# Optimization experiments

Measured on AMD Instinct MI355X. Metric: run time of the kernel, lower is better.

## Reference

```python
import jax, jax.numpy as jnp
import numpy as np

N_NODES = 32768
N_EDGES = 524288
NODE_DIM = 128
HIDDEN = 256
EDGE_DIM = 32


def setup_inputs() -> dict:
    key = jax.random.key(0)
    ks = jax.random.split(key, 12)
    s = 0.05
    return {
        "h": jax.random.normal(ks[0], (N_NODES, NODE_DIM), jnp.float32),
        "x": jax.random.normal(ks[1], (N_NODES, 3), jnp.float32) * 10.0,
        "edge_index": jax.random.randint(ks[2], (2, N_EDGES), 0, N_NODES, dtype=jnp.int32).astype(jnp.int64),
        "edge_dist": jax.random.uniform(ks[3], (N_EDGES,), jnp.float32) * 15.0,
        # edge_mlp: Linear(1, edge_dim) -> SiLU -> Linear(edge_dim, edge_dim)
        "We1": jax.random.normal(ks[4], (1, EDGE_DIM), jnp.float32) * s,
        "be1": jnp.zeros((EDGE_DIM,), jnp.float32),
        "We2": jax.random.normal(ks[5], (EDGE_DIM, EDGE_DIM), jnp.float32) * s,
        "be2": jnp.zeros((EDGE_DIM,), jnp.float32),
        # node_mlp: Linear(2*node+edge, hidden) -> SiLU -> Linear(hidden, node)
        "Wn1": jax.random.normal(ks[6], (2 * NODE_DIM + EDGE_DIM, HIDDEN), jnp.float32) * s,
        "bn1": jnp.zeros((HIDDEN,), jnp.float32),
        "Wn2": jax.random.normal(ks[7], (HIDDEN, NODE_DIM), jnp.float32) * s,
        "bn2": jnp.zeros((NODE_DIM,), jnp.float32),
        # coord_mlp: Linear(2*node+edge, hidden) -> SiLU -> Linear(hidden, 1, bias=False)
        "Wc1": jax.random.normal(ks[8], (2 * NODE_DIM + EDGE_DIM, HIDDEN), jnp.float32) * s,
        "bc1": jnp.zeros((HIDDEN,), jnp.float32),
        "Wc2": jax.random.normal(ks[9], (HIDDEN, 1), jnp.float32) * s,
    }


def reference(h, x, edge_index, edge_dist,
              We1, be1, We2, be2,
              Wn1, bn1, Wn2, bn2,
              Wc1, bc1, Wc2):
    src, dst = edge_index[0], edge_index[1]
    n_nodes = h.shape[0]

    # edge_mlp on scalar distances -> [E, edge_dim]
    edge_attr = jax.nn.silu(edge_dist[:, None] @ We1 + be1) @ We2 + be2

    # per-edge message input: [E, 2*node_dim + edge_dim]
    m_input = jnp.concatenate([h[src], h[dst], edge_attr], axis=-1)

    # node messages and scatter-add onto destination nodes
    m = jax.nn.silu(m_input @ Wn1 + bn1) @ Wn2 + bn2          # [E, node_dim]
    h_agg = jax.ops.segment_sum(m, dst, num_segments=n_nodes)  # [N, node_dim]

    # equivariant coordinate update along normalized edge direction
    coord_weight = jax.nn.silu(m_input @ Wc1 + bc1) @ Wc2      # [E, 1]
    dir_vec = x[src] - x[dst]                                  # [E, 3]
    dir_len = jnp.maximum(jnp.linalg.norm(dir_vec, axis=-1, keepdims=True), 1e-8)
    coord_update = coord_weight * (dir_vec / dir_len)          # [E, 3]
    x_agg = jax.ops.segment_sum(coord_update, dst, num_segments=n_nodes)

    return h + h_agg, x + x_agg
```

## Files before the change

### kernel.cpp

```cpp
#include <hip/hip_runtime.h>
#include <math.h>

#define N_NODES 32768
#define N_EDGES 524288
#define NODE_DIM 128
#define HIDDEN 256
#define EDGE_DIM 32
#define TE 64
#define ASTR 296
#define HSTR 264
#define MSTR 132

typedef __attribute__((ext_vector_type(8))) short bf16x8;
typedef __attribute__((ext_vector_type(16))) float f32x16;

__device__ __forceinline__ float silu_f(float v) {
    float e = __expf(-v);
    return v * __builtin_amdgcn_rcpf(1.0f + e);
}

__device__ __forceinline__ unsigned short f2bf_rne(float f) {
    union { float f; unsigned int u; } v; v.f = f;
    return (unsigned short)((v.u + 0x7fffu + ((v.u >> 16) & 1u)) >> 16);
}
__device__ __forceinline__ unsigned int pk_rne(float a, float b) {
    return (unsigned int)f2bf_rne(a) | ((unsigned int)f2bf_rne(b) << 16);
}
__device__ __forceinline__ unsigned int pkbf(float a, float b) {
    union { float f; unsigned int u; } ua, ub; ua.f = a; ub.f = b;
    return __builtin_amdgcn_perm(ub.u + 0x8000u, ua.u + 0x8000u, 0x07060302u);
}
__device__ __forceinline__ unsigned short f2bf_hu(float f) {
    union { float f; unsigned int u; } v; v.f = f;
    return (unsigned short)((v.u + 0x8000u) >> 16);
}

__device__ __forceinline__ int detect_is64(const void* ei, int t) {
    const unsigned int* ew = (const unsigned int*)ei;
    unsigned int hiw = ew[2 * (t & 63) + 1];
    return (__ballot(hiw != 0u) == 0ULL) ? 1 : 0;
}

#define WS_BIAS_OFF 1024
#define WS_W1S_OFF  69632
#define WS_W2S_OFF  364544
#define WS_CNT_OFF  430080
#define WS_CUR_OFF  561152
#define WS_PERM_OFF 692224
#define WS_PART_OFF 2789376
#define WS_HBF_OFF  2790400
#define WS_HBF_END  (WS_HBF_OFF + N_NODES * NODE_DIM * 2)

#define SEG_CNT  32768
#define SEG_W1S  147456
#define SEG_W2S  32768
#define SEG_BIAS 512
#define SEG_OUT  1073152
#define SEG_HBF  524288
#define PREP_TOT (SEG_CNT + SEG_W1S + SEG_W2S + SEG_BIAS + SEG_OUT + SEG_HBF)

__global__ void prep_all_kernel(const float* __restrict__ h, const float* __restrict__ x,
                                const float* __restrict__ We2, const float* __restrict__ be2,
                                const float* __restrict__ Wn1, const float* __restrict__ bn1,
                                const float* __restrict__ Wn2,
                                const float* __restrict__ Wc1, const float* __restrict__ bc1,
                                float* __restrict__ out, float* __restrict__ biasC,
                                unsigned short* __restrict__ W1s, unsigned short* __restrict__ W2s,
                                int* __restrict__ counts, unsigned short* __restrict__ hbf) {
    int i = blockIdx.x * 256 + threadIdx.x;
    if (i < SEG_CNT) { counts[i] = 0; return; }
    i -= SEG_CNT;
    if (i < SEG_W1S) {
        int jj = i & 7, ln = (i >> 3) & 63, rest = i >> 9;
        int step = rest % 18, tile = rest / 18;
        int n = tile * 32 + (ln & 31);
        int k = step * 16 + ((ln >> 5) * 8) + jj;
        float v;
        if (k < 256) {
            v = (n < 256) ? Wn1[k * 256 + n] : Wc1[k * 256 + (n - 256)];
        } else {
            int j = k - 256;
            float s = 0.0f;
            #pragma unroll 8
            for (int q = 0; q < 32; ++q)
                s += We2[j * 32 + q] * ((n < 256) ? Wn1[(256 + q) * 256 + n]
                                                  : Wc1[(256 + q) * 256 + (n - 256)]);
            v = s;
        }
        W1s[i] = f2bf_rne(v);
        return;
    }
    i -= SEG_W1S;
    if (i < SEG_W2S) {
        int jj = i & 7, ln = (i >> 3) & 63, rest = i >> 9;
        int step = rest & 15, tile = rest >> 4;
        int d = tile * 32 + (ln & 31);
        int k = step * 16 + ((ln >> 5) * 8) + jj;
        W2s[i] = f2bf_rne(Wn2[k * 128 + d]);
        return;
    }
    i -= SEG_W2S;
    if (i < SEG_BIAS) {
        int n = i;
        float s = (n < 256) ? bn1[n] : bc1[n - 256];
        #pragma unroll 8
        for (int q = 0; q < 32; ++q)
            s += be2[q] * ((n < 256) ? Wn1[(256 + q) * 256 + n]
                                     : Wc1[(256 + q) * 256 + (n - 256)]);
        biasC[n] = s;
        return;
    }
    i -= SEG_BIAS;
    if (i < SEG_OUT) {
        const int NH4 = N_NODES * NODE_DIM / 4;
        const float4* h4 = (const float4*)h;
        const float4* x4 = (const float4*)x;
        ((float4*)out)[i] = (i < NH4) ? h4[i] : x4[i - NH4];
        return;
    }
    i -= SEG_OUT;
    if (hbf != nullptr && i < SEG_HBF) {
        const float4* p = (const float4*)&h[i * 8];
        float4 v0 = p[0], v1 = p[1];
        uint4 o = make_uint4(pk_rne(v0.x, v0.y), pk_rne(v0.z, v0.w),
                             pk_rne(v1.x, v1.y), pk_rne(v1.z, v1.w));
        *(uint4*)&hbf[i * 8] = o;
    }
}

__global__ void hist_kernel(const void* __restrict__ ei, int* __restrict__ counts) {
    int is64 = detect_is64(ei, threadIdx.x);
    int e = blockIdx.x * 256 + threadIdx.x;
    int dst = is64 ? (int)((const long long*)ei)[N_EDGES + e]
                   : ((const int*)ei)[N_EDGES + e];
    atomicAdd(&counts[dst], 1);
}

__global__ __launch_bounds__(256)
void scanA_kernel(const int* __restrict__ counts, int* __restrict__ partials) {
    __shared__ int red[256];
    const int t = threadIdx.x;
    const int b = blockIdx.x;
    red[t] = counts[b * 256 + t];
    __syncthreads();
    #pragma unroll
    for (int s = 128; s > 0; s >>= 1) {
        if (t < s) red[t] += red[t + s];
        __syncthreads();
    }
    if (t == 0) partials[b] = red[0];
}

__global__ __launch_bounds__(256)
void scanC_kernel(const int* __restrict__ counts, const int* __restrict__ partials,
                  int* __restrict__ cursor) {
    __shared__ int pb[128];
    __shared__ int loc[256];
    const int t = threadIdx.x;
    const int b = blockIdx.x;
    if (t < 128) pb[t] = partials[t];
    int c = counts[b * 256 + t];
    loc[t] = c;
    __syncthreads();
    if (t == 0) {
        int s = 0;
        for (int j = 0; j < 128; ++j) { int v = pb[j]; pb[j] = s; s += v; }
    }
    #pragma unroll
    for (int d = 1; d < 256; d <<= 1) {
        int v = (t >= d) ? loc[t - d] : 0;
        __syncthreads();
        loc[t] += v;
        __syncthreads();
    }
    cursor[b * 256 + t] = pb[b] + loc[t] - c;
}

__global__ void place_kernel(const void* __restrict__ ei,
                             int* __restrict__ cursor, int* __restrict__ perm) {
    int is64 = detect_is64(ei, threadIdx.x);
    int e = blockIdx.x * 256 + threadIdx.x;
    int dst = is64 ? (int)((const long long*)ei)[N_EDGES + e]
                   : ((const int*)ei)[N_EDGES + e];
    int pos = atomicAdd(&cursor[dst], 1);
    perm[pos] = e;
}

__global__ __launch_bounds__(512, 4)
void egnn_mfma_kernel(const float* __restrict__ h, const float* __restrict__ x,
                      const void* __restrict__ ei, const float* __restrict__ dist,
                      const float* __restrict__ We1, const float* __restrict__ be1,
                      const float* __restrict__ bn2, const float* __restrict__ Wc2,
                      const float* __restrict__ biasC,
                      const unsigned short* __restrict__ W1s,
                      const unsigned short* __restrict__ W2s,
                      const int* __restrict__ perm,
                      const unsigned short* __restrict__ hbf,
                      float* __restrict__ out)
{
    __shared__ unsigned short smA[TE * ASTR];
    __shared__ int sidx[TE], didx[TE], eidx[TE];
    __shared__ float cw_s[TE];
    __shared__ float cxyz[3 * TE];

    unsigned short* smH = smA;
    float* smM = (float*)smA;

    const int t = threadIdx.x;
    const int lane = t & 63;
    const int wv = t >> 6;
    const int lo = lane & 31;
    const int hi = lane >> 5;
    const int ebase = blockIdx.x * TE;
    const int is64 = detect_is64(ei, t);

    if (t < 2 * TE) {
        int e = t & (TE - 1);
        int eid = perm[ebase + e];
        int which = t >> 6;
        long long pos = (long long)which * N_EDGES + eid;
        int idx = is64 ? (int)((const long long*)ei)[pos] : ((const int*)ei)[pos];
        if (which == 0) { sidx[e] = idx; eidx[e] = eid; }
        else didx[e] = idx;
        if (t < TE) cw_s[t] = 0.0f;
    }
    __syncthreads();

    if (hbf != nullptr) {
        #pragma unroll
        for (int it = 0; it < 4; ++it) {
            int id = it * 512 + t;
            int g = id & 15;
            int half = (id >> 4) & 1;
            int e = id >> 5;
            int node = half ? didx[e] : sidx[e];
            uint4 v = *(const uint4*)&hbf[node * NODE_DIM + 8 * g];
            *(uint4*)&smA[e * ASTR + half * NODE_DIM + 8 * g] = v;
        }
    } else {
        #pragma unroll
        for (int it = 0; it < 4; ++it) {
            int id = it * 512 + t;
            int g8 = id & 15;
            int half = (id >> 4) & 1;
            int e = id >> 5;
            int node = half ? didx[e] : sidx[e];
            const float4* p = (const float4*)&h[node * NODE_DIM + 8 * g8];
            float4 v0 = p[0], v1 = p[1];
            unsigned int a0 = pkbf(v0.x, v0.y), a1 = pkbf(v0.z, v0.w);
            unsigned int a2 = pkbf(v1.x, v1.y), a3 = pkbf(v1.z, v1.w);
            *(uint4*)&smA[e * ASTR + half * NODE_DIM + 8 * g8] = make_uint4(a0, a1, a2, a3);
        }
    }
    {
        int e = t >> 3;
        int j4 = (t & 7) * 4;
        float d = dist[eidx[e]];
        float s0 = silu_f(d * We1[j4 + 0] + be1[j4 + 0]);
        float s1 = silu_f(d * We1[j4 + 1] + be1[j4 + 1]);
        float s2 = silu_f(d * We1[j4 + 2] + be1[j4 + 2]);
        float s3 = silu_f(d * We1[j4 + 3] + be1[j4 + 3]);
        *(uint2*)&smA[e * ASTR + 2 * NODE_DIM + j4] = make_uint2(pkbf(s0, s1), pkbf(s2, s3));
    }
    __syncthreads();

    f32x16 a00, a01, a10, a11;
    {
        int nb = wv * 64 + lo;
        float b0 = biasC[nb], b1 = biasC[nb + 32];
        #pragma unroll
        for (int r = 0; r < 16; ++r) { a00[r] = b0; a01[r] = b1; a10[r] = b0; a11[r] = b1; }
    }
    {
        const int aoff0 = lo * ASTR + hi * 8;
        const int aoff1 = (32 + lo) * ASTR + hi * 8;
        const int TS = 18 * 64 * 8;
        const int base = ((wv * 2 * 18) * 64 + lane) * 8;
        bf16x8 b0s[3], b1s[3];
        b0s[0] = *(const bf16x8*)&W1s[base];
        b1s[0] = *(const bf16x8*)&W1s[base + TS];
        b0s[1] = *(const bf16x8*)&W1s[base + 512];
        b1s[1] = *(const bf16x8*)&W1s[base + 512 + TS];
        #pragma unroll
        for (int step = 0; step < 18; ++step) {
            const int cur = step % 3;
            if (step + 2 < 18) {
                const int pf = (step + 2) % 3;
                b0s[pf] = *(const bf16x8*)&W1s[base + (step + 2) * 512];
                b1s[pf] = *(const bf16x8*)&W1s[base + (step + 2) * 512 + TS];
            }
            bf16x8 f0 = *(const bf16x8*)&smA[aoff0 + step * 16];
            bf16x8 f1 = *(const bf16x8*)&smA[aoff1 + step * 16];
            a00 = __builtin_amdgcn_mfma_f32_32x32x16_bf16(f0, b0s[cur], a00, 0, 0, 0);
            a10 = __builtin_amdgcn_mfma_f32_32x32x16_bf16(f1, b0s[cur], a10, 0, 0, 0);
            a01 = __builtin_amdgcn_mfma_f32_32x32x16_bf16(f0, b1s[cur], a01, 0, 0, 0);
            a11 = __builtin_amdgcn_mfma_f32_32x32x16_bf16(f1, b1s[cur], a11, 0, 0, 0);
        }
    }
    __syncthreads();

    const int rowbase = 4 * hi;
    if (wv < 4) {
        int jb = wv * 64 + lo;
        #pragma unroll
        for (int r = 0; r < 16; ++r) {
            int er = (r & 3) + 8 * (r >> 2) + rowbase;
            unsigned short* row0 = &smH[er * HSTR + jb];
            unsigned short* row1 = &smH[(er + 32) * HSTR + jb];
            row0[0]  = f2bf_hu(silu_f(a00[r]));
            row0[32] = f2bf_hu(silu_f(a01[r]));
            row1[0]  = f2bf_hu(silu_f(a10[r]));
            row1[32] = f2bf_hu(silu_f(a11[r]));
        }
    } else {
        int nc = (wv - 4) * 64 + lo;
        float w0 = Wc2[nc], w1 = Wc2[nc + 32];
        float p0[16], p1[16];
        #pragma unroll
        for (int r = 0; r < 16; ++r) {
            p0[r] = silu_f(a00[r]) * w0 + silu_f(a01[r]) * w1;
            p1[r] = silu_f(a10[r]) * w0 + silu_f(a11[r]) * w1;
        }
        #pragma unroll
        for (int off = 1; off < 32; off <<= 1) {
            #pragma unroll
            for (int r = 0; r < 16; ++r) {
                p0[r] += __shfl_xor(p0[r], off);
                p1[r] += __shfl_xor(p1[r], off);
            }
        }
        if (lo == 0) {
            #pragma unroll
            for (int r = 0; r < 16; ++r) {
                int er = (r & 3) + 8 * (r >> 2) + rowbase;
                atomicAdd(&cw_s[er], p0[r]);
                atomicAdd(&cw_s[er + 32], p1[r]);
            }
        }
    }
    __syncthreads();

    if (t < TE) {
        int s = sidx[t], dn = didx[t];
        float dx = x[s * 3 + 0] - x[dn * 3 + 0];
        float dy = x[s * 3 + 1] - x[dn * 3 + 1];
        float dz = x[s * 3 + 2] - x[dn * 3 + 2];
        float len = fmaxf(sqrtf(dx * dx + dy * dy + dz * dz), 1e-8f);
        float w = cw_s[t] / len;
        cxyz[t] = w * dx; cxyz[TE + t] = w * dy; cxyz[2 * TE + t] = w * dz;
    }

    {
        const int et = wv >> 2;
        const int dt = wv & 3;
        const int d = dt * 32 + lo;
        f32x16 acc;
        float bb = bn2[d];
        #pragma unroll
        for (int r = 0; r < 16; ++r) acc[r] = bb;
        const int hoff = (et * 32 + lo) * HSTR + hi * 8;
        const int wb = ((dt * 16) * 64 + lane) * 8;
        bf16x8 bs[3];
        bs[0] = *(const bf16x8*)&W2s[wb];
        bs[1] = *(const bf16x8*)&W2s[wb + 512];
        #pragma unroll
        for (int step = 0; step < 16; ++step) {
            const int cur = step % 3;
            if (step + 2 < 16) {
                const int pf = (step + 2) % 3;
                bs[pf] = *(const bf16x8*)&W2s[wb + (step + 2) * 512];
            }
            bf16x8 af = *(const bf16x8*)&smH[hoff + step * 16];
            acc = __builtin_amdgcn_mfma_f32_32x32x16_bf16(af, bs[cur], acc, 0, 0, 0);
        }
        __syncthreads();
        #pragma unroll
        for (int r = 0; r < 16; ++r) {
            int er = et * 32 + (r & 3) + 8 * (r >> 2) + rowbase;
            smM[er * MSTR + d] = acc[r];
        }
    }
    __syncthreads();

    {
        const int g = t >> 5;
        const int d4 = (t & 31) * 4;
        for (int e0 = g; e0 < TE; e0 += 16) {
            if (e0 > 0 && didx[e0] == didx[e0 - 1]) continue;
            float4 s = *(const float4*)&smM[e0 * MSTR + d4];
            int er = e0 + 1;
            while (er < TE && didx[er] == didx[e0]) {
                float4 v = *(const float4*)&smM[er * MSTR + d4];
                s.x += v.x; s.y += v.y; s.z += v.z; s.w += v.w;
                ++er;
            }
            float* dp = &out[didx[e0] * NODE_DIM + d4];
            atomicAdd(dp + 0, s.x); atomicAdd(dp + 1, s.y);
            atomicAdd(dp + 2, s.z); atomicAdd(dp + 3, s.w);
        }
    }
    if (t < TE) {
        int e0 = t;
        if (e0 == 0 || didx[e0] != didx[e0 - 1]) {
            float sx = cxyz[e0], sy = cxyz[TE + e0], sz = cxyz[2 * TE + e0];
            int er = e0 + 1;
            while (er < TE && didx[er] == didx[e0]) {
                sx += cxyz[er]; sy += cxyz[TE + er]; sz += cxyz[2 * TE + er];
                ++er;
            }
            float* xo = out + N_NODES * NODE_DIM + didx[e0] * 3;
            atomicAdd(xo + 0, sx); atomicAdd(xo + 1, sy); atomicAdd(xo + 2, sz);
        }
    }
}

extern "C" void kernel_launch(void* const* d_in, const int* in_sizes, int n_in,
                              void* d_out, int out_size, void* d_ws, size_t ws_size,
                              hipStream_t stream) {
    const float* h    = (const float*)d_in[0];
    const float* x    = (const float*)d_in[1];
    const void*  ei   = d_in[2];
    const float* dist = (const float*)d_in[3];
    const float* We1  = (const float*)d_in[4];
    const float* be1  = (const float*)d_in[5];
    const float* We2  = (const float*)d_in[6];
    const float* be2  = (const float*)d_in[7];
    const float* Wn1  = (const float*)d_in[8];
    const float* bn1  = (const float*)d_in[9];
    const float* Wn2  = (const float*)d_in[10];
    const float* bn2  = (const float*)d_in[11];
    const float* Wc1  = (const float*)d_in[12];
    const float* bc1  = (const float*)d_in[13];
    const float* Wc2  = (const float*)d_in[14];
    float* out = (float*)d_out;

    float* biasC = (float*)((char*)d_ws + WS_BIAS_OFF);
    unsigned short* W1s = (unsigned short*)((char*)d_ws + WS_W1S_OFF);
    unsigned short* W2s = (unsigned short*)((char*)d_ws + WS_W2S_OFF);
    int* counts   = (int*)((char*)d_ws + WS_CNT_OFF);
    int* cursor   = (int*)((char*)d_ws + WS_CUR_OFF);
    int* perm     = (int*)((char*)d_ws + WS_PERM_OFF);
    int* partials = (int*)((char*)d_ws + WS_PART_OFF);
    unsigned short* hbf = (ws_size >= (size_t)WS_HBF_END)
                        ? (unsigned short*)((char*)d_ws + WS_HBF_OFF) : nullptr;

    prep_all_kernel<<<PREP_TOT / 256, 256, 0, stream>>>(
        h, x, We2, be2, Wn1, bn1, Wn2, Wc1, bc1,
        out, biasC, W1s, W2s, counts, hbf);

    hist_kernel<<<N_EDGES / 256, 256, 0, stream>>>(ei, counts);
    scanA_kernel<<<128, 256, 0, stream>>>(counts, partials);
    scanC_kernel<<<128, 256, 0, stream>>>(counts, partials, cursor);
    place_kernel<<<N_EDGES / 256, 256, 0, stream>>>(ei, cursor, perm);

    egnn_mfma_kernel<<<N_EDGES / TE, 512, 0, stream>>>(
        h, x, ei, dist, We1, be1, bn2, Wc2, biasC, W1s, W2s, perm, hbf, out);
}
```

Before: 479.7 us.

## Switch to node-owned blocks with shared-memory aggregation instead of global atomics

The main kernel now launches one block per 64 destination nodes. Each block walks its CSR edge range in 64-edge tiles, reusing the existing MFMA message pipeline. Partial sums go into shared-memory accumulators for h and x, and each block writes out = h + agg and x + xagg directly. This removes the global atomic scatter and the separate full-output copy in the prep kernel. In exchange, the grid is much smaller, shared memory per block roughly doubles (lower occupancy), tail tiles run partially filled, and per-block edge counts may be imbalanced.

Measured after the change: 1.383 ms. +188.3%, slower.

```diff
diff --git a/kernel.cpp b/kernel.cpp
--- a/kernel.cpp
+++ b/kernel.cpp
@@ -10,6 +10,7 @@
 #define ASTR 296
 #define HSTR 264
 #define MSTR 132
+#define HACCSTR 132
 
 typedef __attribute__((ext_vector_type(8))) short bf16x8;
 typedef __attribute__((ext_vector_type(16))) float f32x16;
@@ -55,16 +56,15 @@
 #define SEG_W1S  147456
 #define SEG_W2S  32768
 #define SEG_BIAS 512
-#define SEG_OUT  1073152
 #define SEG_HBF  524288
-#define PREP_TOT (SEG_CNT + SEG_W1S + SEG_W2S + SEG_BIAS + SEG_OUT + SEG_HBF)
-
-__global__ void prep_all_kernel(const float* __restrict__ h, const float* __restrict__ x,
+#define PREP_TOT (SEG_CNT + SEG_W1S + SEG_W2S + SEG_BIAS + SEG_HBF)
+
+__global__ void prep_all_kernel(const float* __restrict__ h,
                                 const float* __restrict__ We2, const float* __restrict__ be2,
                                 const float* __restrict__ Wn1, const float* __restrict__ bn1,
                                 const float* __restrict__ Wn2,
                                 const float* __restrict__ Wc1, const float* __restrict__ bc1,
-                                float* __restrict__ out, float* __restrict__ biasC,
+                                float* __restrict__ biasC,
                                 unsigned short* __restrict__ W1s, unsigned short* __restrict__ W2s,
                                 int* __restrict__ counts, unsigned short* __restrict__ hbf) {
     int i = blockIdx.x * 256 + threadIdx.x;
@@ -111,14 +111,6 @@
         return;
     }
     i -= SEG_BIAS;
-    if (i < SEG_OUT) {
-        const int NH4 = N_NODES * NODE_DIM / 4;
-        const float4* h4 = (const float4*)h;
-        const float4* x4 = (const float4*)x;
-        ((float4*)out)[i] = (i < NH4) ? h4[i] : x4[i - NH4];
-        return;
-    }
-    i -= SEG_OUT;
     if (hbf != nullptr && i < SEG_HBF) {
         const float4* p = (const float4*)&h[i * 8];
         float4 v0 = p[0], v1 = p[1];
@@ -187,7 +179,7 @@
 }
 
 __global__ __launch_bounds__(512, 4)
-void egnn_mfma_kernel(const float* __restrict__ h, const float* __restrict__ x,
+void egnn_node_kernel(const float* __restrict__ h, const float* __restrict__ x,
                       const void* __restrict__ ei, const float* __restrict__ dist,
                       const float* __restrict__ We1, const float* __restrict__ be1,
                       const float* __restrict__ bn2, const float* __restrict__ Wc2,
@@ -195,13 +187,16 @@
                       const unsigned short* __restrict__ W1s,
                       const unsigned short* __restrict__ W2s,
                       const int* __restrict__ perm,
+                      const int* __restrict__ counts, const int* __restrict__ cursor,
                       const unsigned short* __restrict__ hbf,
                       float* __restrict__ out)
 {
     __shared__ unsigned short smA[TE * ASTR];
+    __shared__ float hacc[TE * HACCSTR];
     __shared__ int sidx[TE], didx[TE], eidx[TE];
     __shared__ float cw_s[TE];
     __shared__ float cxyz[3 * TE];
+    __shared__ float xacc[3 * TE];
 
     unsigned short* smH = smA;
     float* smM = (float*)smA;
@@ -211,206 +206,234 @@
     const int wv = t >> 6;
     const int lo = lane & 31;
     const int hi = lane >> 5;
-    const int ebase = blockIdx.x * TE;
+    const int nodebase = blockIdx.x * TE;
     const int is64 = detect_is64(ei, t);
 
-    if (t < 2 * TE) {
-        int e = t & (TE - 1);
-        int eid = perm[ebase + e];
-        int which = t >> 6;
-        long long pos = (long long)which * N_EDGES + eid;
-        int idx = is64 ? (int)((const long long*)ei)[pos] : ((const int*)ei)[pos];
-        if (which == 0) { sidx[e] = idx; eidx[e] = eid; }
-        else didx[e] = idx;
-        if (t < TE) cw_s[t] = 0.0f;
-    }
+    const int estart = cursor[nodebase] - counts[nodebase];
+    const int eend   = cursor[nodebase + TE - 1];
+
+    for (int i = t; i < TE * HACCSTR; i += 512) hacc[i] = 0.0f;
+    if (t < 3 * TE) xacc[t] = 0.0f;
     __syncthreads();
 
-    if (hbf != nullptr) {
-        #pragma unroll
-        for (int it = 0; it < 4; ++it) {
-            int id = it * 512 + t;
-            int g = id & 15;
-            int half = (id >> 4) & 1;
-            int e = id >> 5;
-            int node = half ? didx[e] : sidx[e];
-            uint4 v = *(const uint4*)&hbf[node * NODE_DIM + 8 * g];
-            *(uint4*)&smA[e * ASTR + half * NODE_DIM + 8 * g] = v;
-        }
-    } else {
-        #pragma unroll
-        for (int it = 0; it < 4; ++it) {
-            int id = it * 512 + t;
-            int g8 = id & 15;
-            int half = (id >> 4) & 1;
-            int e = id >> 5;
-            int node = half ? didx[e] : sidx[e];
-            const float4* p = (const float4*)&h[node * NODE_DIM + 8 * g8];
-            float4 v0 = p[0], v1 = p[1];
-            unsigned int a0 = pkbf(v0.x, v0.y), a1 = pkbf(v0.z, v0.w);
-            unsigned int a2 = pkbf(v1.x, v1.y), a3 = pkbf(v1.z, v1.w);
-            *(uint4*)&smA[e * ASTR + half * NODE_DIM + 8 * g8] = make_uint4(a0, a1, a2, a3);
-        }
-    }
-    {
-        int e = t >> 3;
-        int j4 = (t & 7) * 4;
-        float d = dist[eidx[e]];
-        float s0 = silu_f(d * We1[j4 + 0] + be1[j4 + 0]);
-        float s1 = silu_f(d * We1[j4 + 1] + be1[j4 + 1]);
-        float s2 = silu_f(d * We1[j4 + 2] + be1[j4 + 2]);
-        float s3 = silu_f(d * We1[j4 + 3] + be1[j4 + 3]);
-        *(uint2*)&smA[e * ASTR + 2 * NODE_DIM + j4] = make_uint2(pkbf(s0, s1), pkbf(s2, s3));
-    }
-    __syncthreads();
-
-    f32x16 a00, a01, a10, a11;
-    {
-        int nb = wv * 64 + lo;
-        float b0 = biasC[nb], b1 = biasC[nb + 32];
-        #pragma unroll
-        for (int r = 0; r < 16; ++r) { a00[r] = b0; a01[r] = b1; a10[r] = b0; a11[r] = b1; }
-    }
-    {
-        const int aoff0 = lo * ASTR + hi * 8;
-        const int aoff1 = (32 + lo) * ASTR + hi * 8;
-        const int TS = 18 * 64 * 8;
-        const int base = ((wv * 2 * 18) * 64 + lane) * 8;
-        bf16x8 b0s[3], b1s[3];
-        b0s[0] = *(const bf16x8*)&W1s[base];
-        b1s[0] = *(const bf16x8*)&W1s[base + TS];
-        b0s[1] = *(const bf16x8*)&W1s[base + 512];
-        b1s[1] = *(const bf16x8*)&W1s[base + 512 + TS];
-        #pragma unroll
-        for (int step = 0; step < 18; ++step) {
-            const int cur = step % 3;
-            if (step + 2 < 18) {
-                const int pf = (step + 2) % 3;
-                b0s[pf] = *(const bf16x8*)&W1s[base + (step + 2) * 512];
-                b1s[pf] = *(const bf16x8*)&W1s[base + (step + 2) * 512 + TS];
-            }
-            bf16x8 f0 = *(const bf16x8*)&smA[aoff0 + step * 16];
-            bf16x8 f1 = *(const bf16x8*)&smA[aoff1 + step * 16];
-            a00 = __builtin_amdgcn_mfma_f32_32x32x16_bf16(f0, b0s[cur], a00, 0, 0, 0);
-            a10 = __builtin_amdgcn_mfma_f32_32x32x16_bf16(f1, b0s[cur], a10, 0, 0, 0);
-            a01 = __builtin_amdgcn_mfma_f32_32x32x16_bf16(f0, b1s[cur], a01, 0, 0, 0);
-            a11 = __builtin_amdgcn_mfma_f32_32x32x16_bf16(f1, b1s[cur], a11, 0, 0, 0);
-        }
-    }
-    __syncthreads();
-
-    const int rowbase = 4 * hi;
-    if (wv < 4) {
-        int jb = wv * 64 + lo;
-        #pragma unroll
-        for (int r = 0; r < 16; ++r) {
-            int er = (r & 3) + 8 * (r >> 2) + rowbase;
-            unsigned short* row0 = &smH[er * HSTR + jb];
-            unsigned short* row1 = &smH[(er + 32) * HSTR + jb];
-            row0[0]  = f2bf_hu(silu_f(a00[r]));
-            row0[32] = f2bf_hu(silu_f(a01[r]));
-            row1[0]  = f2bf_hu(silu_f(a10[r]));
-            row1[32] = f2bf_hu(silu_f(a11[r]));
-        }
-    } else {
-        int nc = (wv - 4) * 64 + lo;
-        float w0 = Wc2[nc], w1 = Wc2[nc + 32];
-        float p0[16], p1[16];
-        #pragma unroll
-        for (int r = 0; r < 16; ++r) {
-            p0[r] = silu_f(a00[r]) * w0 + silu_f(a01[r]) * w1;
-            p1[r] = silu_f(a10[r]) * w0 + silu_f(a11[r]) * w1;
-        }
-        #pragma unroll
-        for (int off = 1; off < 32; off <<= 1) {
-            #pragma unroll
-            for (int r = 0; r < 16; ++r) {
-                p0[r] += __shfl_xor(p0[r], off);
-                p1[r] += __shfl_xor(p1[r], off);
-            }
-        }
-        if (lo == 0) {
+    for (int tbase = estart; tbase < eend; tbase += TE) {
+        const int cnt = min(TE, eend - tbase);
+
+        if (t < 2 * TE) {
+            int e = t & (TE - 1);
+            int eid = perm[tbase + ((e < cnt) ? e : 0)];
+            int which = t >> 6;
+            long long pos = (long long)which * N_EDGES + eid;
+            int idx = is64 ? (int)((const long long*)ei)[pos] : ((const int*)ei)[pos];
+            if (which == 0) { sidx[e] = idx; eidx[e] = eid; }
+            else didx[e] = idx;
+            if (t < TE) cw_s[t] = 0.0f;
+        }
+        __syncthreads();
+
+        if (hbf != nullptr) {
+            #pragma unroll
+            for (int it = 0; it < 4; ++it) {
+                int id = it * 512 + t;
+                int g = id & 15;
+                int half = (id >> 4) & 1;
+                int e = id >> 5;
+                int node = half ? didx[e] : sidx[e];
+                uint4 v = *(const uint4*)&hbf[node * NODE_DIM + 8 * g];
+                *(uint4*)&smA[e * ASTR + half * NODE_DIM + 8 * g] = v;
+            }
+        } else {
+            #pragma unroll
+            for (int it = 0; it < 4; ++it) {
+                int id = it * 512 + t;
+                int g8 = id & 15;
+                int half = (id >> 4) & 1;
+                int e = id >> 5;
+                int node = half ? didx[e] : sidx[e];
+                const float4* p = (const float4*)&h[node * NODE_DIM + 8 * g8];
+                float4 v0 = p[0], v1 = p[1];
+                unsigned int a0 = pkbf(v0.x, v0.y), a1 = pkbf(v0.z, v0.w);
+                unsigned int a2 = pkbf(v1.x, v1.y), a3 = pkbf(v1.z, v1.w);
+                *(uint4*)&smA[e * ASTR + half * NODE_DIM + 8 * g8] = make_uint4(a0, a1, a2, a3);
+            }
+        }
+        {
+            int e = t >> 3;
+            int j4 = (t & 7) * 4;
+            float d = dist[eidx[e]];
+            float s0 = silu_f(d * We1[j4 + 0] + be1[j4 + 0]);
+            float s1 = silu_f(d * We1[j4 + 1] + be1[j4 + 1]);
+            float s2 = silu_f(d * We1[j4 + 2] + be1[j4 + 2]);
+            float s3 = silu_f(d * We1[j4 + 3] + be1[j4 + 3]);
+            *(uint2*)&smA[e * ASTR + 2 * NODE_DIM + j4] = make_uint2(pkbf(s0, s1), pkbf(s2, s3));
+        }
+        __syncthreads();
+
+        f32x16 a00, a01, a10, a11;
+        {
+            int nb = wv * 64 + lo;
+            float b0 = biasC[nb], b1 = biasC[nb + 32];
+            #pragma unroll
+            for (int r = 0; r < 16; ++r) { a00[r] = b0; a01[r] = b1; a10[r] = b0; a11[r] = b1; }
+        }
+        {
+            const int aoff0 = lo * ASTR + hi * 8;
+            const int aoff1 = (32 + lo) * ASTR + hi * 8;
+            const int TS = 18 * 64 * 8;
+            const int base = ((wv * 2 * 18) * 64 + lane) * 8;
+            bf16x8 b0s[3], b1s[3];
+            b0s[0] = *(const bf16x8*)&W1s[base];
+            b1s[0] = *(const bf16x8*)&W1s[base + TS];
+            b0s[1] = *(const bf16x8*)&W1s[base + 512];
+            b1s[1] = *(const bf16x8*)&W1s[base + 512 + TS];
+            #pragma unroll
+            for (int step = 0; step < 18; ++step) {
+                const int cur = step % 3;
+                if (step + 2 < 18) {
+                    const int pf = (step + 2) % 3;
+                    b0s[pf] = *(const bf16x8*)&W1s[base + (step + 2) * 512];
+                    b1s[pf] = *(const bf16x8*)&W1s[base + (step + 2) * 512 + TS];
+                }
+                bf16x8 f0 = *(const bf16x8*)&smA[aoff0 + step * 16];
+                bf16x8 f1 = *(const bf16x8*)&smA[aoff1 + step * 16];
+                a00 = __builtin_amdgcn_mfma_f32_32x32x16_bf16(f0, b0s[cur], a00, 0, 0, 0);
+                a10 = __builtin_amdgcn_mfma_f32_32x32x16_bf16(f1, b0s[cur], a10, 0, 0, 0);
+                a01 = __builtin_amdgcn_mfma_f32_32x32x16_bf16(f0, b1s[cur], a01, 0, 0, 0);
+                a11 = __builtin_amdgcn_mfma_f32_32x32x16_bf16(f1, b1s[cur], a11, 0, 0, 0);
+            }
+        }
+        __syncthreads();
+
+        const int rowbase = 4 * hi;
+        if (wv < 4) {
+            int jb = wv * 64 + lo;
             #pragma unroll
             for (int r = 0; r < 16; ++r) {
                 int er = (r & 3) + 8 * (r >> 2) + rowbase;
-                atomicAdd(&cw_s[er], p0[r]);
-                atomicAdd(&cw_s[er + 32], p1[r]);
-            }
-        }
-    }
-    __syncthreads();
-
-    if (t < TE) {
-        int s = sidx[t], dn = didx[t];
-        float dx = x[s * 3 + 0] - x[dn * 3 + 0];
-        float dy = x[s * 3 + 1] - x[dn * 3 + 1];
-        float dz = x[s * 3 + 2] - x[dn * 3 + 2];
-        float len = fmaxf(sqrtf(dx * dx + dy * dy + dz * dz), 1e-8f);
-        float w = cw_s[t] / len;
-        cxyz[t] = w * dx; cxyz[TE + t] = w * dy; cxyz[2 * TE + t] = w * dz;
+                unsigned short* row0 = &smH[er * HSTR + jb];
+                unsigned short* row1 = &smH[(er + 32) * HSTR + jb];
+                row0[0]  = f2bf_hu(silu_f(a00[r]));
+                row0[32] = f2bf_hu(silu_f(a01[r]));
+                row1[0]  = f2bf_hu(silu_f(a10[r]));
+                row1[32] = f2bf_hu(silu_f(a11[r]));
+            }
+        } else {
+            int nc = (wv - 4) * 64 + lo;
+            float w0 = Wc2[nc], w1 = Wc2[nc + 32];
+            float p0[16], p1[16];
+            #pragma unroll
+            for (int r = 0; r < 16; ++r) {
+                p0[r] = silu_f(a00[r]) * w0 + silu_f(a01[r]) * w1;
+                p1[r] = silu_f(a10[r]) * w0 + silu_f(a11[r]) * w1;
+            }
+            #pragma unroll
+            for (int off = 1; off < 32; off <<= 1) {
+                #pragma unroll
+                for (int r = 0; r < 16; ++r) {
+                    p0[r] += __shfl_xor(p0[r], off);
+                    p1[r] += __shfl_xor(p1[r], off);
+                }
+            }
+            if (lo == 0) {
+                #pragma unroll
+                for (int r = 0; r < 16; ++r) {
+                    int er = (r & 3) + 8 * (r >> 2) + rowbase;
+                    atomicAdd(&cw_s[er], p0[r]);
+                    atomicAdd(&cw_s[er + 32], p1[r]);
+                }
+            }
+        }
+        __syncthreads();
+
+        if (t < TE) {
+            int s = sidx[t], dn = didx[t];
+            float dx = x[s * 3 + 0] - x[dn * 3 + 0];
+            float dy = x[s * 3 + 1] - x[dn * 3 + 1];
+            float dz = x[s * 3 + 2] - x[dn * 3 + 2];
+            float len = fmaxf(sqrtf(dx * dx + dy * dy + dz * dz), 1e-8f);
+            float w = cw_s[t] / len;
+            cxyz[t] = w * dx; cxyz[TE + t] = w * dy; cxyz[2 * TE + t] = w * dz;
+        }
+
+        {
+            const int et = wv >> 2;
+            const int dt = wv & 3;
+            const int d = dt * 32 + lo;
+            f32x16 acc;
+            float bb = bn2[d];
+            #pragma unroll
+            for (int r = 0; r < 16; ++r) acc[r] = bb;
+            const int hoff = (et * 32 + lo) * HSTR + hi * 8;
+            const int wb = ((dt * 16) * 64 + lane) * 8;
+            bf16x8 bs[3];
+            bs[0] = *(const bf16x8*)&W2s[wb];
+            bs[1] = *(const bf16x8*)&W2s[wb + 512];
+            #pragma unroll
+            for (int step = 0; step < 16; ++step) {
+                const int cur = step % 3;
+                if (step + 2 < 16) {
+                    const int pf = (step + 2) % 3;
+                    bs[pf] = *(const bf16x8*)&W2s[wb + (step + 2) * 512];
+                }
+                bf16x8 af = *(const bf16x8*)&smH[hoff + step * 16];
+                acc = __builtin_amdgcn_mfma_f32_32x32x16_bf16(af, bs[cur], acc, 0, 0, 0);
+            }
+            __syncthreads();
+            #pragma unroll
+            for (int r = 0; r < 16; ++r) {
+                int er = et * 32 + (r & 3) + 8 * (r >> 2) + rowbase;
+                smM[er * MSTR + d] = acc[r];
+            }
+        }
+        __syncthreads();
+
+        {
+            const int g = t >> 5;
+            const int d4 = (t & 31) * 4;
+            for (int e0 = g; e0 < cnt; e0 += 16) {
+                if (e0 > 0 && didx[e0] == didx[e0 - 1]) continue;
+                float4 s = *(const float4*)&smM[e0 * MSTR + d4];
+                int er = e0 + 1;
+                while (er < cnt && didx[er] == didx[e0]) {
+                    float4 v = *(const float4*)&smM[er * MSTR + d4];
+                    s.x += v.x; s.y += v.y; s.z += v.z; s.w += v.w;
+                    ++er;
+                }
+                float* hp = &hacc[(didx[e0] - nodebase) * HACCSTR + d4];
+                hp[0] += s.x; hp[1] += s.y; hp[2] += s.z; hp[3] += s.w;
+            }
+        }
+        if (t < cnt) {
+            int e0 = t;
+            if (e0 == 0 || didx[e0] != didx[e0 - 1]) {
+                float sx = cxyz[e0], sy = cxyz[TE + e0], sz = cxyz[2 * TE + e0];
+                int er = e0 + 1;
+                while (er < cnt && didx[er] == didx[e0]) {
+                    sx += cxyz[er]; sy += cxyz[TE + er]; sz += cxyz[2 * TE + er];
+                    ++er;
+                }
+                int ln = didx[e0] - nodebase;
+                xacc[ln * 3 + 0] += sx; xacc[ln * 3 + 1] += sy; xacc[ln * 3 + 2] += sz;
+            }
+        }
+        __syncthreads();
     }
 
     {
-        const int et = wv >> 2;
-        const int dt = wv & 3;
-        const int d = dt * 32 + lo;
-        f32x16 acc;
-        float bb = bn2[d];
+        const int row = t >> 3;
+        const int c16 = (t & 7) * 16;
+        const float* hp = &h[(nodebase + row) * NODE_DIM + c16];
+        const float* ap = &hacc[row * HACCSTR + c16];
+        float* op = &out[(nodebase + row) * NODE_DIM + c16];
         #pragma unroll
-        for (int r = 0; r < 16; ++r) acc[r] = bb;
-        const int hoff = (et * 32 + lo) * HSTR + hi * 8;
-        const int wb = ((dt * 16) * 64 + lane) * 8;
-        bf16x8 bs[3];
-        bs[0] = *(const bf16x8*)&W2s[wb];
-        bs[1] = *(const bf16x8*)&W2s[wb + 512];
-        #pragma unroll
-        for (int step = 0; step < 16; ++step) {
-            const int cur = step % 3;
-            if (step + 2 < 16) {
-                const int pf = (step + 2) % 3;
-                bs[pf] = *(const bf16x8*)&W2s[wb + (step + 2) * 512];
-            }
-            bf16x8 af = *(const bf16x8*)&smH[hoff + step * 16];
-            acc = __builtin_amdgcn_mfma_f32_32x32x16_bf16(af, bs[cur], acc, 0, 0, 0);
-        }
-        __syncthreads();
-        #pragma unroll
-        for (int r = 0; r < 16; ++r) {
-            int er = et * 32 + (r & 3) + 8 * (r >> 2) + rowbase;
-            smM[er * MSTR + d] = acc[r];
-        }
-    }
-    __syncthreads();
-
-    {
-        const int g = t >> 5;
-        const int d4 = (t & 31) * 4;
-        for (int e0 = g; e0 < TE; e0 += 16) {
-            if (e0 > 0 && didx[e0] == didx[e0 - 1]) continue;
-            float4 s = *(const float4*)&smM[e0 * MSTR + d4];
-            int er = e0 + 1;
-            while (er < TE && didx[er] == didx[e0]) {
-                float4 v = *(const float4*)&smM[er * MSTR + d4];
-                s.x += v.x; s.y += v.y; s.z += v.z; s.w += v.w;
-                ++er;
-            }
-            float* dp = &out[didx[e0] * NODE_DIM + d4];
-            atomicAdd(dp + 0, s.x); atomicAdd(dp + 1, s.y);
-            atomicAdd(dp + 2, s.z); atomicAdd(dp + 3, s.w);
-        }
-    }
-    if (t < TE) {
-        int e0 = t;
-        if (e0 == 0 || didx[e0] != didx[e0 - 1]) {
-            float sx = cxyz[e0], sy = cxyz[TE + e0], sz = cxyz[2 * TE + e0];
-            int er = e0 + 1;
-            while (er < TE && didx[er] == didx[e0]) {
-                sx += cxyz[er]; sy += cxyz[TE + er]; sz += cxyz[2 * TE + er];
-                ++er;
-            }
-            float* xo = out + N_NODES * NODE_DIM + didx[e0] * 3;
-            atomicAdd(xo + 0, sx); atomicAdd(xo + 1, sy); atomicAdd(xo + 2, sz);
-        }
+        for (int j = 0; j < 4; ++j) {
+            float4 hv = ((const float4*)hp)[j];
+            float4 av = *(const float4*)&ap[4 * j];
+            ((float4*)op)[j] = make_float4(hv.x + av.x, hv.y + av.y, hv.z + av.z, hv.w + av.w);
+        }
+    }
+    if (t < 3 * TE) {
+        out[N_NODES * NODE_DIM + nodebase * 3 + t] = x[nodebase * 3 + t] + xacc[t];
     }
 }
 
@@ -445,14 +468,14 @@
                         ? (unsigned short*)((char*)d_ws + WS_HBF_OFF) : nullptr;
 
     prep_all_kernel<<<PREP_TOT / 256, 256, 0, stream>>>(
-        h, x, We2, be2, Wn1, bn1, Wn2, Wc1, bc1,
-        out, biasC, W1s, W2s, counts, hbf);
+        h, We2, be2, Wn1, bn1, Wn2, Wc1, bc1, biasC, W1s, W2s, counts, hbf);
 
     hist_kernel<<<N_EDGES / 256, 256, 0, stream>>>(ei, counts);
     scanA_kernel<<<128, 256, 0, stream>>>(counts, partials);
     scanC_kernel<<<128, 256, 0, stream>>>(counts, partials, cursor);
     place_kernel<<<N_EDGES / 256, 256, 0, stream>>>(ei, cursor, perm);
 
-    egnn_mfma_kernel<<<N_EDGES / TE, 512, 0, stream>>>(
-        h, x, ei, dist, We1, be1, bn2, Wc2, biasC, W1s, W2s, perm, hbf, out);
-}
+    egnn_node_kernel<<<N_NODES / TE, 512, 0, stream>>>(
+        h, x, ei, dist, We1, be1, bn2, Wc2, biasC, W1s, W2s,
+        perm, counts, cursor, hbf, out);
+}
```
